# Optimization experiments

Measured on AMD Instinct MI355X. Metric: run time of the kernel, lower is better.

Reference implementation:

```python
import jax, jax.numpy as jnp
import numpy as np

B, N, C, H, D, M = 8, 4096, 512, 8, 64, 16
TOPK = 3
TAU = 0.1
DIV_REG = 0.01


def setup_inputs() -> dict:
    key = jax.random.key(0)
    ks = jax.random.split(key, 12)
    w = lambda i, shape: 0.02 * jax.random.normal(ks[i], shape, dtype=jnp.float32)
    return {
        "x": jax.random.normal(ks[0], (B, N, C), dtype=jnp.float32),
        "W_qkv": w(1, (C, 3 * C)),                    # qkv_bias=False
        "W_proj": w(2, (C, C)), "b_proj": jnp.zeros((C,), jnp.float32),
        "W_rspec": w(3, (C, H * M)), "b_rspec": jnp.zeros((H * M,), jnp.float32),
        "W_rspat": w(4, (C, H * M)), "b_rspat": jnp.zeros((H * M,), jnp.float32),
        "K_spec": w(5, (H, M, D)),                    # prototype banks (EMA buffers)
        "K_spat": w(6, (H, M, D)),
        "W_tok": w(7, (D, D)), "b_tok": jnp.zeros((D,), jnp.float32),
        "W_prot": w(8, (D, D)), "b_prot": jnp.zeros((D,), jnp.float32),
    }


def topk_mask_from_logits(logits, k):
    # keep top-k of softmax probs along last axis, renormalize
    vals = jax.lax.top_k(logits, k)[0]
    thresh = vals[..., -1:]
    mask = (logits >= thresh).astype(logits.dtype)
    probs = jax.nn.softmax(logits, axis=-1) * mask
    denom = jnp.maximum(jnp.sum(probs, axis=-1, keepdims=True), 1e-6)
    return probs / denom


def _l2norm(a, eps):
    return a / jnp.maximum(jnp.linalg.norm(a, axis=-1, keepdims=True), eps)


def reference(x, W_qkv, W_proj, b_proj, W_rspec, b_rspec, W_rspat, b_rspat,
              K_spec, K_spat, W_tok, b_tok, W_prot, b_prot):
    # qkv: [B,N,3C] -> q,k,v each [B,H,N,D]
    qkv = (x @ W_qkv).reshape(B, N, 3, H, D).transpose(2, 0, 3, 1, 4)
    q, _k, v = qkv[0], qkv[1], qkv[2]

    # routing logits [B,H,N,M] -> top-k masked probs
    r_spec = topk_mask_from_logits(
        (x @ W_rspec + b_rspec).reshape(B, N, H, M).transpose(0, 2, 1, 3), TOPK)
    r_spat = topk_mask_from_logits(
        (x @ W_rspat + b_rspat).reshape(B, N, H, M).transpose(0, 2, 1, 3), TOPK)

    # effective keys from prototype banks: [B,H,N,D]
    K_eff = (jnp.einsum('bhnm,hmd->bhnd', r_spec, K_spec)
             + jnp.einsum('bhnm,hmd->bhnd', r_spat, K_spat))
    K_norm = jax.nn.softmax(K_eff, axis=-2)          # softmax over tokens N

    # linear attention reorder: context [B,H,D,D], then Q @ context
    context = jnp.einsum('bhnd,bhne->bhde', K_norm, v)
    out = jnp.einsum('bhnd,bhde->bhne', q, context)  # note: scale unused in source
    out = out.transpose(0, 2, 1, 3).reshape(B, N, C) @ W_proj + b_proj

    # ---- contrastive aux loss ----
    t_n = _l2norm(v @ W_tok + b_tok, 1e-12)          # [B,H,N,D]
    p_spec_n = _l2norm(K_spec @ W_prot + b_prot, 1e-12)
    p_spat_n = _l2norm(K_spat @ W_prot + b_prot, 1e-12)
    sim_spec = jnp.einsum('bhnd,hmd->bhnm', t_n, p_spec_n)
    sim_spat = jnp.einsum('bhnd,hmd->bhnm', t_n, p_spat_n)
    pos_spec = jnp.sum(sim_spec * r_spec, axis=-1)
    pos_spat = jnp.sum(sim_spat * r_spat, axis=-1)
    loss_spec = -jnp.mean(pos_spec / TAU - jax.nn.logsumexp(sim_spec / TAU, axis=-1))
    loss_spat = -jnp.mean(pos_spat / TAU - jax.nn.logsumexp(sim_spat / TAU, axis=-1))
    contrastive_loss = 0.5 * (loss_spec + loss_spat)

    def diversity_loss(P):
        h, m, _d = P.shape
        p = P / jnp.maximum(jnp.linalg.norm(P, axis=-1, keepdims=True), 1e-6)
        sim = jnp.einsum('hmd,hnd->hmn', p, p)
        mask = 1.0 - jnp.eye(m, dtype=P.dtype)[None]
        return jnp.sum(sim * mask) / (h * m * (m - 1) + 1e-6)

    diversity = DIV_REG * (diversity_loss(K_spec) + diversity_loss(K_spat))
    return out, contrastive_loss, diversity
```

## Files before the change

kernel.cpp:

```cpp
#include <hip/hip_runtime.h>
#include <math.h>

#define B_ 8
#define N_ 4096
#define C_ 512
#define H_ 8
#define D_ 64
#define M_ 16
#define BN_TOK (B_*N_)
#define TAU_ 0.1f

typedef short s8v __attribute__((ext_vector_type(8)));
typedef float f4v __attribute__((ext_vector_type(4)));
typedef unsigned short u16;

__device__ __forceinline__ float wave_reduce_sum(float v){
  #pragma unroll
  for (int o = 32; o > 0; o >>= 1) v += __shfl_xor(v, o);
  return v;
}

__device__ __forceinline__ unsigned short f2b(float f){
  unsigned int u = __float_as_uint(f);
  u += 0x7fffu + ((u >> 16) & 1u);
  return (unsigned short)(u >> 16);
}

__device__ __forceinline__ float b2f(u16 b){
  return __uint_as_float(((unsigned int)b) << 16);
}

__device__ __forceinline__ s8v pack8(const float* f){
  s8v r;
  #pragma unroll
  for (int e = 0; e < 8; ++e) r[e] = (short)f2b(f[e]);
  return r;
}

__device__ __forceinline__ void gload16(const u16* g, u16* l){
  __builtin_amdgcn_global_load_lds(
      (const __attribute__((address_space(1))) unsigned int*)g,
      (__attribute__((address_space(3))) unsigned int*)l, 16, 0, 0);
}

__global__ __launch_bounds__(256) void prep_all(const float* __restrict__ x, u16* __restrict__ xb,
                                                const float* __restrict__ W_qkv,
                                                const float* __restrict__ W_rspec,
                                                const float* __restrict__ W_rspat,
                                                const float* __restrict__ W_proj,
                                                u16* __restrict__ Wqk,
                                                u16* __restrict__ Wt_v,
                                                u16* __restrict__ Wt_r,
                                                u16* __restrict__ Wt_p){
  const int bid = blockIdx.x;
  const int t = threadIdx.x;
  if (bid < 1024) {
    const int n8 = (BN_TOK*C_)/8;
    for (int i = bid * 256 + t; i < n8; i += 1024*256) {
      const float4* p = (const float4*)(x + (size_t)i * 8);
      float4 a = p[0], b = p[1];
      float f[8] = {a.x,a.y,a.z,a.w,b.x,b.y,b.z,b.w};
      *(s8v*)(xb + (size_t)i * 8) = pack8(f);
    }
    return;
  }
  if (bid < 1536) {
    const int k = bid - 1024;
    Wqk[(size_t)k*512 + t]       = f2b(W_qkv[(size_t)k*1536 + t]);
    Wqk[(size_t)k*512 + t + 256] = f2b(W_qkv[(size_t)k*1536 + t + 256]);
    return;
  }
  const int r = bid - 1536;
  const float* src; int ld, coff, n; u16* dst;
  if (r < 512)       { src = W_qkv;   ld = 1536; coff = 1024; n = r;        dst = Wt_v; }
  else if (r < 640)  { src = W_rspec; ld = 128;  coff = 0;    n = r - 512;  dst = Wt_r; }
  else if (r < 768)  { src = W_rspat; ld = 128;  coff = 0;    n = r - 640;  dst = Wt_r + 128*512; }
  else               { src = W_proj;  ld = 512;  coff = 0;    n = r - 768;  dst = Wt_p; }
  dst[(size_t)n*512 + t]       = f2b(src[(size_t)t*ld + coff + n]);
  dst[(size_t)n*512 + t + 256] = f2b(src[(size_t)(t+256)*ld + coff + n]);
}

template<int MODE>
__global__ __launch_bounds__(256) void gemm_bt(const u16* __restrict__ A,
                                               const u16* __restrict__ Bt,
                                               const float* __restrict__ bias,
                                               void* __restrict__ C,
                                               int K, int lda, int ldc, int bt_bstride) {
  __shared__ __align__(16) u16 Asm[2][2][128*32];
  __shared__ __align__(16) u16 Bsm[2][2][128*32];
  const int tid = threadIdx.x;
  const int lane = tid & 63, w = tid >> 6;
  const int bm = blockIdx.x * 128, bn = blockIdx.y * 128;

  const int lrow = lane >> 2;
  const int kch  = ((lane & 3) ^ ((lane >> 3) & 3)) << 3;

  const u16* Btb = Bt + (size_t)(bm >> 12) * bt_bstride;
  const u16* Ag0 = A   + (size_t)(bm + w*16 + lrow) * lda + kch;
  const u16* Ag1 = Ag0 + (size_t)64 * lda;
  const u16* Bg0 = Btb + (size_t)(bn + w*16 + lrow) * K + kch;
  const u16* Bg1 = Bg0 + (size_t)64 * K;
  const int l0 = (w*16)*32, l1 = (w*16+64)*32;

  const int lm = lane & 15, lg = lane >> 4;
  const int w0 = (w >> 1) * 64, c0 = (w & 1) * 64;
  const int xs = (lg ^ ((lm >> 1) & 3)) << 3;

  const int NSTEP = K >> 6;

  f4v acc[4][4];
  #pragma unroll
  for (int i = 0; i < 4; ++i)
    #pragma unroll
    for (int j = 0; j < 4; ++j) acc[i][j] = (f4v){0.f,0.f,0.f,0.f};

  #define STAGE(buf, tt)                                        \
    gload16(Ag0 + (tt)*64,      &Asm[buf][0][l0]);              \
    gload16(Ag1 + (tt)*64,      &Asm[buf][0][l1]);              \
    gload16(Ag0 + (tt)*64 + 32, &Asm[buf][1][l0]);              \
    gload16(Ag1 + (tt)*64 + 32, &Asm[buf][1][l1]);              \
    gload16(Bg0 + (tt)*64,      &Bsm[buf][0][l0]);              \
    gload16(Bg1 + (tt)*64,      &Bsm[buf][0][l1]);              \
    gload16(Bg0 + (tt)*64 + 32, &Bsm[buf][1][l0]);              \
    gload16(Bg1 + (tt)*64 + 32, &Bsm[buf][1][l1]);

  STAGE(0, 0)
  STAGE(1, 1)

  int cur = 0;
  for (int k = 0; k < NSTEP; ++k) {
    if (k < NSTEP - 1) asm volatile("s_waitcnt vmcnt(8)" ::: "memory");
    else               asm volatile("s_waitcnt vmcnt(0)" ::: "memory");
    __builtin_amdgcn_s_barrier();
    __builtin_amdgcn_sched_barrier(0);

    #pragma unroll
    for (int h = 0; h < 2; ++h) {
      s8v af[4], bf_[4];
      #pragma unroll
      for (int i = 0; i < 4; ++i) af[i]  = *(const s8v*)&Asm[cur][h][(w0 + 16*i + lm)*32 + xs];
      #pragma unroll
      for (int j = 0; j < 4; ++j) bf_[j] = *(const s8v*)&Bsm[cur][h][(c0 + 16*j + lm)*32 + xs];
      #pragma unroll
      for (int i = 0; i < 4; ++i)
        #pragma unroll
        for (int j = 0; j < 4; ++j)
          acc[i][j] = __builtin_amdgcn_mfma_f32_16x16x32_bf16(af[i], bf_[j], acc[i][j], 0, 0, 0);
    }

    __builtin_amdgcn_sched_barrier(0);
    __builtin_amdgcn_s_barrier();
    if (k + 2 < NSTEP) {
      STAGE(cur, k + 2)
    }
    __builtin_amdgcn_sched_barrier(0);
    cur ^= 1;
  }
  #undef STAGE

  #pragma unroll
  for (int j = 0; j < 4; ++j) {
    const int col = bn + c0 + 16*j + lm;
    const float bj = (MODE == 0 && bias) ? bias[col] : 0.f;
    #pragma unroll
    for (int i = 0; i < 4; ++i) {
      const int row = bm + w0 + 16*i + 4*lg;
      #pragma unroll
      for (int r = 0; r < 4; ++r) {
        if (MODE == 1) ((u16*)C)[(size_t)(row + r) * ldc + col] = f2b(acc[i][j][r]);
        else           ((float*)C)[(size_t)(row + r) * ldc + col] = acc[i][j][r] + bj;
      }
    }
  }
}

__global__ __launch_bounds__(256) void router_topk(const float* __restrict__ logits,
                            const float* __restrict__ b_rspec, const float* __restrict__ b_rspat,
                            float* __restrict__ r_spec, float* __restrict__ r_spat,
                            u16* __restrict__ rb_spec, u16* __restrict__ rb_spat) {
  int t = blockIdx.x * blockDim.x + threadIdx.x;
  if (t >= BN_TOK * H_ * 2) return;
  int route = t & 1, h = (t >> 1) & 7, bn = t >> 4;
  int b = bn >> 12, n = bn & 4095;
  const float* lg = logits + (size_t)bn*256 + route*128 + h*16;
  const float* bias = (route ? b_rspat : b_rspec) + h*16;
  float v[16];
  #pragma unroll
  for (int m=0;m<16;++m) v[m] = lg[m] + bias[m];
  float m1=-1e30f, m2=-1e30f, m3=-1e30f;
  #pragma unroll
  for (int m=0;m<16;++m){
    float x=v[m];
    if (x>m1){m3=m2;m2=m1;m1=x;}
    else if (x>m2){m3=m2;m2=x;}
    else if (x>m3){m3=x;}
  }
  float S=0.f, Sm=0.f, e[16];
  #pragma unroll
  for (int m=0;m<16;++m){ e[m]=expf(v[m]-m1); S+=e[m]; if (v[m]>=m3) Sm+=e[m]; }
  float denom = fmaxf(Sm/S, 1e-6f);
  float inv = 1.f/(S*denom);
  size_t idx = (((size_t)b*H_ + h)*N_ + n)*16;
  float* r = (route ? r_spat : r_spec) + idx;
  u16* rb  = (route ? rb_spat : rb_spec) + idx;
  #pragma unroll
  for (int m=0;m<16;++m) {
    float val = (v[m] >= m3) ? e[m]*inv : 0.f;
    r[m] = val;
    rb[m] = f2b(val);
  }
}

__global__ __launch_bounds__(256) void context_mfma(const u16* __restrict__ rb_spec, const u16* __restrict__ rb_spat,
                               const float* __restrict__ K_spec, const float* __restrict__ K_spat,
                               const u16* __restrict__ vb, float* __restrict__ pctx, float* __restrict__ pZ) {
  const int chunk = blockIdx.x & 15, bh = blockIdx.x >> 4;
  const int b = bh >> 3, h = bh & 7;
  const int tid = threadIdx.x;
  const int lane = tid & 63, w = tid >> 6;
  const int lm = lane & 15, lg = lane >> 4;

  __shared__ __align__(16) unsigned short Kc[64*32];
  __shared__ __align__(16) unsigned short Rs[64*32];
  __shared__ __align__(16) unsigned short Vt[64*64];
  __shared__ __align__(16) unsigned short Ps[64*64];
  __shared__ float Zs[256];

  {
    int d = tid & 63, c = tid >> 6;
    float f[8];
    #pragma unroll
    for (int u = 0; u < 8; ++u) {
      int k = c*8 + u;
      f[u] = (k < 16) ? K_spec[h*1024 + k*64 + d] : K_spat[h*1024 + (k-16)*64 + d];
    }
    *(s8v*)&Kc[d*32 + ((c ^ (d&3)) << 3)] = pack8(f);
  }

  const u16* rsg = rb_spec + ((size_t)bh*N_ + chunk*256)*16;
  const u16* rtg = rb_spat + ((size_t)bh*N_ + chunk*256)*16;
  const u16* vbase = vb + h*64;
  const size_t tokbase = (size_t)b*N_ + chunk*256;

  f4v acc2[4];
  #pragma unroll
  for (int j = 0; j < 4; ++j) acc2[j] = (f4v){0.f,0.f,0.f,0.f};
  float zreg[4] = {0.f,0.f,0.f,0.f};

  for (int t0 = 0; t0 < 4; ++t0) {
    __syncthreads();
    {
      int n = tid & 63, c = tid >> 6;
      const u16* src = (c < 2 ? rsg : rtg) + ((size_t)(t0*64 + n))*16 + (c&1)*8;
      *(s8v*)&Rs[n*32 + ((c ^ (n&3)) << 3)] = *(const s8v*)src;
    }
    {
      int n = tid & 63, eq = tid >> 6;
      const u16* src = vbase + (tokbase + t0*64 + n)*512 + eq*16;
      u16 f[16];
      *(s8v*)&f[0] = ((const s8v*)src)[0];
      *(s8v*)&f[8] = ((const s8v*)src)[1];
      #pragma unroll
      for (int u = 0; u < 16; ++u) {
        int e = eq*16 + u;
        Vt[e*64 + ((((n>>3) ^ (e&7)) << 3) | (n&7))] = f[u];
      }
    }
    __syncthreads();
    {
      s8v a1 = *(const s8v*)&Rs[(16*w + lm)*32 + ((lg ^ (lm&3)) << 3)];
      #pragma unroll
      for (int j = 0; j < 4; ++j) {
        s8v b1 = *(const s8v*)&Kc[(16*j + lm)*32 + ((lg ^ (lm&3)) << 3)];
        f4v c1 = (f4v){0.f,0.f,0.f,0.f};
        c1 = __builtin_amdgcn_mfma_f32_16x16x32_bf16(a1, b1, c1, 0, 0, 0);
        float p0 = expf(c1[0]), p1 = expf(c1[1]), p2 = expf(c1[2]), p3 = expf(c1[3]);
        float zz = p0 + p1 + p2 + p3;
        zz += __shfl_xor(zz, 16); zz += __shfl_xor(zz, 32);
        zreg[j] += zz;
        int d = 16*j + lm;
        int n0w = 16*w + 4*lg;
        Ps[d*64 + (((((n0w  )>>3) ^ (d&7)) << 3) | ((n0w  )&7))] = f2b(p0);
        Ps[d*64 + (((((n0w+1)>>3) ^ (d&7)) << 3) | ((n0w+1)&7))] = f2b(p1);
        Ps[d*64 + (((((n0w+2)>>3) ^ (d&7)) << 3) | ((n0w+2)&7))] = f2b(p2);
        Ps[d*64 + (((((n0w+3)>>3) ^ (d&7)) << 3) | ((n0w+3)&7))] = f2b(p3);
      }
    }
    __syncthreads();
    #pragma unroll
    for (int kb = 0; kb < 2; ++kb) {
      s8v a2 = *(const s8v*)&Vt[(16*w + lm)*64 + (((kb*4 + lg) ^ (lm&7)) << 3)];
      #pragma unroll
      for (int j = 0; j < 4; ++j) {
        s8v b2 = *(const s8v*)&Ps[(16*j + lm)*64 + (((kb*4 + lg) ^ (lm&7)) << 3)];
        acc2[j] = __builtin_amdgcn_mfma_f32_16x16x32_bf16(a2, b2, acc2[j], 0, 0, 0);
      }
    }
  }
  float* pc = pctx + (size_t)(bh*16 + chunk)*4096;
  #pragma unroll
  for (int j = 0; j < 4; ++j) {
    #pragma unroll
    for (int r = 0; r < 4; ++r)
      pc[(16*w + 4*lg + r)*64 + 16*j + lm] = acc2[j][r];
    if (lg == 0) Zs[w*64 + 16*j + lm] = zreg[j];
  }
  __syncthreads();
  if (tid < 64)
    pZ[(size_t)(bh*16 + chunk)*64 + tid] = Zs[tid] + Zs[64+tid] + Zs[128+tid] + Zs[192+tid];
}

__global__ __launch_bounds__(256) void context_reduce(const float* __restrict__ pctx, const float* __restrict__ pZ,
                              float* __restrict__ ctx) {
  const int gid = blockIdx.x * 256 + threadIdx.x;
  const int bh = gid >> 12, e = (gid >> 6) & 63, d = gid & 63;
  float z = 0.f, s = 0.f;
  for (int c = 0; c < 16; ++c) {
    z += pZ[(size_t)(bh*16 + c)*64 + d];
    s += pctx[(size_t)(bh*16 + c)*4096 + e*64 + d];
  }
  ctx[(size_t)bh*4096 + e*64 + d] = s / z;
}

__global__ __launch_bounds__(256) void cwt_kernel(const float* __restrict__ ctx, const u16* __restrict__ Wt_p,
                                                  u16* __restrict__ CWt) {
  const int bh = blockIdx.x >> 3, oct = blockIdx.x & 7;
  const int b = bh >> 3, h = bh & 7;
  const int tid = threadIdx.x;
  __shared__ float ctxS[64*64];
  __shared__ u16 WsL[64*64];
  {
    int e = tid >> 2, dq = tid & 3;
    const float4* src = (const float4*)(ctx + (size_t)bh*4096 + e*64 + dq*16);
    float4* dst = (float4*)(ctxS + e*64 + dq*16);
    dst[0] = src[0]; dst[1] = src[1]; dst[2] = src[2]; dst[3] = src[3];
  }
  const int c0 = oct * 64;
  {
    int cl = tid >> 2, eq = tid & 3;
    const s8v* src = (const s8v*)(Wt_p + (size_t)(c0 + cl)*512 + h*64 + eq*16);
    *(s8v*)&WsL[cl*64 + eq*16]     = src[0];
    *(s8v*)&WsL[cl*64 + eq*16 + 8] = src[1];
  }
  __syncthreads();
  const int d = tid & 63, cq = tid >> 6;
  for (int ci = 0; ci < 16; ++ci) {
    int cl = cq*16 + ci;
    float acc = 0.f;
    #pragma unroll
    for (int e = 0; e < 64; ++e)
      acc = fmaf(ctxS[e*64 + d], b2f(WsL[cl*64 + e]), acc);
    CWt[((size_t)b*512 + (c0 + cl))*512 + h*64 + d] = f2b(acc);
  }
}

__global__ __launch_bounds__(64) void protnorm_div(const float* __restrict__ K_spec, const float* __restrict__ K_spat,
                               const float* __restrict__ W_prot, const float* __restrict__ b_prot,
                               float* __restrict__ pnorm, float* __restrict__ pdiv) {
  const int bid = blockIdx.x;
  const int e = threadIdx.x;
  if (bid < 256) {
    int route = bid >> 7, hm = bid & 127;
    const float* Km = (route ? K_spat : K_spec) + hm*64;
    __shared__ float kv[64];
    kv[e] = Km[e];
    __syncthreads();
    float acc = b_prot[e];
    for (int dcol = 0; dcol < 64; ++dcol) acc = fmaf(kv[dcol], W_prot[dcol*64 + e], acc);
    float n2 = wave_reduce_sum(acc*acc);
    pnorm[(size_t)bid*64 + e] = acc / fmaxf(sqrtf(n2), 1e-12f);
    return;
  }
  const int db = bid - 256;
  int route = db >> 3, h = db & 7;
  const float* Km = (route ? K_spat : K_spec) + h*16*64;
  float s = 0.f, selfsum = 0.f;
  for (int m = 0; m < 16; ++m) {
    float x = Km[m*64 + e];
    float n2 = wave_reduce_sum(x*x);
    float p = x / fmaxf(sqrtf(n2), 1e-6f);
    s += p; selfsum += p*p;
  }
  float off = wave_reduce_sum(s*s - selfsum);
  if (e == 0) pdiv[db] = off;
}

__global__ __launch_bounds__(256) void contrastive_mfma(const u16* __restrict__ vb,
                                   const float* __restrict__ r_spec, const float* __restrict__ r_spat,
                                   const float* __restrict__ W_tok, const float* __restrict__ b_tok,
                                   const float* __restrict__ pnorm, float* __restrict__ pcontr) {
  const int tile = blockIdx.x & 255;
  const int h = blockIdx.x >> 8;
  const int t0 = tile * 128;
  const int b = t0 >> 12;
  const int n0 = t0 & 4095;
  const int tid = threadIdx.x;
  const int lane = tid & 63, w = tid >> 6;
  const int lm = lane & 15, lg = lane >> 4;

  __shared__ __align__(16) unsigned short Usm[128*72];
  __shared__ __align__(16) unsigned short Wsm[64*72];
  __shared__ __align__(16) unsigned short Psm[32*72];
  __shared__ float nrmS[128];
  __shared__ float btkS[64];
  __shared__ float bred[2][4];
  float* Uf = (float*)Usm;

  {
    const int vr = tid >> 1, vh = tid & 1;
    const u16* vg = vb + (size_t)(b*N_ + n0 + vr)*512 + h*64 + vh*32;
    #pragma unroll
    for (int c = 0; c < 4; ++c) *(s8v*)&Usm[vr*72 + vh*32 + c*8] = ((const s8v*)vg)[c];
  }
  {
    const int e = tid & 63, kh = tid >> 6;
    float f[16];
    #pragma unroll
    for (int rr = 0; rr < 16; ++rr) f[rr] = W_tok[(size_t)(kh*16+rr)*64 + e];
    *(s8v*)&Wsm[e*72 + kh*16]     = pack8(&f[0]);
    *(s8v*)&Wsm[e*72 + kh*16 + 8] = pack8(&f[8]);
  }
  if (tid < 128) {
    const int proto = tid >> 2, q4 = tid & 3;
    const int src = (proto < 16) ? (h*16 + proto) : (128 + h*16 + (proto-16));
    const float* pg = pnorm + (size_t)src*64 + q4*16;
    float f[16];
    #pragma unroll
    for (int i = 0; i < 4; ++i) {
      float4 v4 = ((const float4*)pg)[i];
      f[4*i]=v4.x; f[4*i+1]=v4.y; f[4*i+2]=v4.z; f[4*i+3]=v4.w;
    }
    *(s8v*)&Psm[proto*72 + q4*16]     = pack8(&f[0]);
    *(s8v*)&Psm[proto*72 + q4*16 + 8] = pack8(&f[8]);
  }
  if (tid < 64) btkS[tid] = b_tok[tid];
  __syncthreads();

  f4v acc[2][4];
  #pragma unroll
  for (int i=0;i<2;++i)
    #pragma unroll
    for (int j=0;j<4;++j) acc[i][j] = (f4v){0.f,0.f,0.f,0.f};
  {
    s8v bf0[4], bf1[4];
    #pragma unroll
    for (int j=0;j<4;++j) {
      bf0[j] = *(const s8v*)&Wsm[(j*16+lm)*72 + lg*8];
      bf1[j] = *(const s8v*)&Wsm[(j*16+lm)*72 + 32 + lg*8];
    }
    #pragma unroll
    for (int i=0;i<2;++i) {
      s8v af0 = *(const s8v*)&Usm[(w*32+16*i+lm)*72 + lg*8];
      s8v af1 = *(const s8v*)&Usm[(w*32+16*i+lm)*72 + 32 + lg*8];
      #pragma unroll
      for (int j=0;j<4;++j) {
        acc[i][j] = __builtin_amdgcn_mfma_f32_16x16x32_bf16(af0, bf0[j], acc[i][j], 0, 0, 0);
        acc[i][j] = __builtin_amdgcn_mfma_f32_16x16x32_bf16(af1, bf1[j], acc[i][j], 0, 0, 0);
      }
    }
  }
  #pragma unroll
  for (int i=0;i<2;++i) {
    #pragma unroll
    for (int r=0;r<4;++r) {
      float s = 0.f;
      #pragma unroll
      for (int j=0;j<4;++j) {
        float val = acc[i][j][r] + btkS[j*16+lm];
        acc[i][j][r] = val;
        s += val*val;
      }
      s += __shfl_xor(s,1); s += __shfl_xor(s,2); s += __shfl_xor(s,4); s += __shfl_xor(s,8);
      if (lm == 0) nrmS[w*32 + 16*i + lg*4 + r] = s;
    }
  }
  #pragma unroll
  for (int i=0;i<2;++i)
    #pragma unroll
    for (int j=0;j<4;++j)
      #pragma unroll
      for (int r=0;r<4;++r)
        Usm[(w*32+16*i+lg*4+r)*72 + j*16+lm] = f2b(acc[i][j][r]);
  __syncthreads();

  f4v acc2[2][2];
  #pragma unroll
  for (int i=0;i<2;++i)
    #pragma unroll
    for (int j=0;j<2;++j) acc2[i][j] = (f4v){0.f,0.f,0.f,0.f};
  {
    s8v bf0[2], bf1[2];
    #pragma unroll
    for (int j=0;j<2;++j) {
      bf0[j] = *(const s8v*)&Psm[(j*16+lm)*72 + lg*8];
      bf1[j] = *(const s8v*)&Psm[(j*16+lm)*72 + 32 + lg*8];
    }
    #pragma unroll
    for (int i=0;i<2;++i) {
      s8v af0 = *(const s8v*)&Usm[(w*32+16*i+lm)*72 + lg*8];
      s8v af1 = *(const s8v*)&Usm[(w*32+16*i+lm)*72 + 32 + lg*8];
      #pragma unroll
      for (int j=0;j<2;++j) {
        acc2[i][j] = __builtin_amdgcn_mfma_f32_16x16x32_bf16(af0, bf0[j], acc2[i][j], 0, 0, 0);
        acc2[i][j] = __builtin_amdgcn_mfma_f32_16x16x32_bf16(af1, bf1[j], acc2[i][j], 0, 0, 0);
      }
    }
  }
  #pragma unroll
  for (int i=0;i<2;++i)
    #pragma unroll
    for (int j=0;j<2;++j)
      #pragma unroll
      for (int r=0;r<4;++r)
        Uf[(w*32+16*i+lg*4+r)*36 + j*16+lm] = acc2[i][j][r];
  __syncthreads();

  float l = 0.f;
  {
    const int tt = tid >> 1, route = tid & 1;
    float inv = 1.f / fmaxf(sqrtf(nrmS[tt]), 1e-12f);
    const float* rg = (route ? r_spat : r_spec) + (((size_t)b*H_ + h)*N_ + n0 + tt)*16;
    float s0[16];
    #pragma unroll
    for (int m=0;m<16;++m) s0[m] = Uf[tt*36 + route*16 + m]*inv;
    float pos = 0.f, mx = -1e30f;
    #pragma unroll
    for (int m=0;m<16;++m) {
      pos += s0[m]*rg[m];
      mx = fmaxf(mx, s0[m]);
    }
    float z = 0.f;
    #pragma unroll
    for (int m=0;m<16;++m) z += expf((s0[m]-mx)/TAU_);
    l = pos/TAU_ - (mx/TAU_ + logf(z));
  }
  float lspec = (tid & 1) ? 0.f : l;
  float lspat = (tid & 1) ? l : 0.f;
  lspec = wave_reduce_sum(lspec);
  lspat = wave_reduce_sum(lspat);
  if (lane == 0) { bred[0][w]=lspec; bred[1][w]=lspat; }
  __syncthreads();
  if (tid == 0) {
    pcontr[2*blockIdx.x]     = bred[0][0]+bred[0][1]+bred[0][2]+bred[0][3];
    pcontr[2*blockIdx.x + 1] = bred[1][0]+bred[1][1]+bred[1][2]+bred[1][3];
  }
}

__global__ __launch_bounds__(256) void finalize_kernel(const float* __restrict__ pcontr,
                                                       const float* __restrict__ pdiv,
                                                       float* __restrict__ tail) {
  __shared__ float red[2][4];
  const int tid = threadIdx.x, lane = tid & 63, w = tid >> 6;
  float ls = 0.f, lt = 0.f;
  for (int k = tid; k < 2048; k += 256) { ls += pcontr[2*k]; lt += pcontr[2*k + 1]; }
  ls = wave_reduce_sum(ls);
  lt = wave_reduce_sum(lt);
  if (lane == 0) { red[0][w] = ls; red[1][w] = lt; }
  __syncthreads();
  if (tid == 0) {
    float sspec = red[0][0]+red[0][1]+red[0][2]+red[0][3];
    float sspat = red[1][0]+red[1][1]+red[1][2]+red[1][3];
    float dspec = 0.f, dspat = 0.f;
    for (int k = 0; k < 8; ++k) { dspec += pdiv[k]; dspat += pdiv[8+k]; }
    float loss_spec = -(sspec / (float)(B_*H_*N_));
    float loss_spat = -(sspat / (float)(B_*H_*N_));
    float denom = (float)(H_*M_*(M_-1)) + 1e-6f;
    tail[0] = 0.5f*(loss_spec + loss_spat);
    tail[1] = 0.01f * (dspec/denom + dspat/denom);
  }
}

extern "C" void kernel_launch(void* const* d_in, const int* in_sizes, int n_in,
                              void* d_out, int out_size, void* d_ws, size_t ws_size,
                              hipStream_t stream) {
  const float* x       = (const float*)d_in[0];
  const float* W_qkv   = (const float*)d_in[1];
  const float* W_proj  = (const float*)d_in[2];
  const float* b_proj  = (const float*)d_in[3];
  const float* W_rspec = (const float*)d_in[4];
  const float* b_rspec = (const float*)d_in[5];
  const float* W_rspat = (const float*)d_in[6];
  const float* b_rspat = (const float*)d_in[7];
  const float* K_spec  = (const float*)d_in[8];
  const float* K_spat  = (const float*)d_in[9];
  const float* W_tok   = (const float*)d_in[10];
  const float* b_tok   = (const float*)d_in[11];
  const float* W_prot  = (const float*)d_in[12];
  const float* b_prot  = (const float*)d_in[13];
  float* out = (float*)d_out;

  float* ws = (float*)d_ws;
  u16*   vb      = (u16*)ws;
  float* logits  = ws + 8388608;
  float* pctx    = ws + 8388608;
  float* pZ      = ws + 8388608 + 4194304;
  float* r_spec  = ws + 16777216;
  float* r_spat  = ws + 20971520;
  u16*   rb_spec = (u16*)(ws + 25165824);
  u16*   rb_spat = (u16*)(ws + 27262976);
  u16*   xb      = (u16*)(ws + 29360128);
  u16*   Wqk     = (u16*)(ws + 37748736);
  u16*   Wt_v    = (u16*)(ws + 37879808);
  u16*   Wt_r    = (u16*)(ws + 38010880);
  u16*   Wt_p    = (u16*)(ws + 38076416);
  float* ctxb    = ws + 38207488;
  float* pnorm   = ws + 38469632;
  float* pcontr  = ws + 38486016;
  float* pdiv    = ws + 38490112;
  u16*   CWt     = (u16*)(ws + 38490128);
  u16*   W2t     = (u16*)(ws + 39538704);

  dim3 blk256(256);

  prep_all<<<2816, blk256, 0, stream>>>(x, xb, W_qkv, W_rspec, W_rspat, W_proj, Wqk, Wt_v, Wt_r, Wt_p);

  gemm_bt<0><<<dim3(256,2), blk256, 0, stream>>>(xb, Wt_r, nullptr, logits, 512, 512, 256, 0);
  router_topk<<<2048, blk256, 0, stream>>>(logits, b_rspec, b_rspat, r_spec, r_spat, rb_spec, rb_spat);
  gemm_bt<1><<<dim3(256,4), blk256, 0, stream>>>(xb, Wt_v, nullptr, vb, 512, 512, 512, 0);
  context_mfma<<<1024, blk256, 0, stream>>>(rb_spec, rb_spat, K_spec, K_spat, vb, pctx, pZ);
  context_reduce<<<1024, blk256, 0, stream>>>(pctx, pZ, ctxb);
  cwt_kernel<<<512, blk256, 0, stream>>>(ctxb, Wt_p, CWt);
  gemm_bt<1><<<dim3(32,4), blk256, 0, stream>>>(CWt, Wqk, nullptr, W2t, 512, 512, 512, 0);
  protnorm_div<<<272, dim3(64), 0, stream>>>(K_spec, K_spat, W_prot, b_prot, pnorm, pdiv);
  contrastive_mfma<<<2048, blk256, 0, stream>>>(vb, r_spec, r_spat, W_tok, b_tok, pnorm, pcontr);
  gemm_bt<0><<<dim3(256,4), blk256, 0, stream>>>(xb, W2t, b_proj, out, 512, 512, 512, 512*512);
  finalize_kernel<<<1, blk256, 0, stream>>>(pcontr, pdiv, out + 16777216);
}
```

Baseline: 323.0 us.

## Fuse router-logit and V projections into one GEMM; drop fp32 routing probs

Adds a GEMM mode that writes the first columns of the output as bf16 V and the remaining columns as fp32 router logits, so the V projection and the router-logit projection run as one launch over a 6-column-tile grid. The router kernel no longer writes fp32 routing probabilities, and the contrastive kernel reads the bf16 copies instead. This saves a kernel launch, one pass over the activations, and a large fp32 write and read. In exchange the routing weights in the positive-similarity term now carry bf16 rounding. It also relies on the transposed router weights sitting directly after the V weights in the workspace.

```diff
diff --git a/kernel.cpp b/kernel.cpp
--- a/kernel.cpp
+++ b/kernel.cpp
@@ -85,7 +85,9 @@
                                                const u16* __restrict__ Bt,
                                                const float* __restrict__ bias,
                                                void* __restrict__ C,
-                                               int K, int lda, int ldc, int bt_bstride) {
+                                               float* __restrict__ C2,
+                                               int K, int lda, int ldc, int ldc2,
+                                               int split, int bt_bstride) {
   __shared__ __align__(16) u16 Asm[2][2][128*32];
   __shared__ __align__(16) u16 Bsm[2][2][128*32];
   const int tid = threadIdx.x;
@@ -158,6 +160,7 @@
   }
   #undef STAGE
 
+  const bool tobf = (MODE == 1) || (MODE == 2 && bn < split);
   #pragma unroll
   for (int j = 0; j < 4; ++j) {
     const int col = bn + c0 + 16*j + lm;
@@ -167,8 +170,9 @@
       const int row = bm + w0 + 16*i + 4*lg;
       #pragma unroll
       for (int r = 0; r < 4; ++r) {
-        if (MODE == 1) ((u16*)C)[(size_t)(row + r) * ldc + col] = f2b(acc[i][j][r]);
-        else           ((float*)C)[(size_t)(row + r) * ldc + col] = acc[i][j][r] + bj;
+        if (tobf)            ((u16*)C)[(size_t)(row + r) * ldc + col] = f2b(acc[i][j][r]);
+        else if (MODE == 2)  C2[(size_t)(row + r) * ldc2 + (col - split)] = acc[i][j][r];
+        else                 ((float*)C)[(size_t)(row + r) * ldc + col] = acc[i][j][r] + bj;
       }
     }
   }
@@ -176,7 +180,6 @@
 
 __global__ __launch_bounds__(256) void router_topk(const float* __restrict__ logits,
                             const float* __restrict__ b_rspec, const float* __restrict__ b_rspat,
-                            float* __restrict__ r_spec, float* __restrict__ r_spat,
                             u16* __restrict__ rb_spec, u16* __restrict__ rb_spat) {
   int t = blockIdx.x * blockDim.x + threadIdx.x;
   if (t >= BN_TOK * H_ * 2) return;
@@ -201,12 +204,10 @@
   float denom = fmaxf(Sm/S, 1e-6f);
   float inv = 1.f/(S*denom);
   size_t idx = (((size_t)b*H_ + h)*N_ + n)*16;
-  float* r = (route ? r_spat : r_spec) + idx;
   u16* rb  = (route ? rb_spat : rb_spec) + idx;
   #pragma unroll
   for (int m=0;m<16;++m) {
     float val = (v[m] >= m3) ? e[m]*inv : 0.f;
-    r[m] = val;
     rb[m] = f2b(val);
   }
 }
@@ -386,7 +387,7 @@
 }
 
 __global__ __launch_bounds__(256) void contrastive_mfma(const u16* __restrict__ vb,
-                                   const float* __restrict__ r_spec, const float* __restrict__ r_spat,
+                                   const u16* __restrict__ rb_spec, const u16* __restrict__ rb_spat,
                                    const float* __restrict__ W_tok, const float* __restrict__ b_tok,
                                    const float* __restrict__ pnorm, float* __restrict__ pcontr) {
   const int tile = blockIdx.x & 255;
@@ -519,14 +520,14 @@
   {
     const int tt = tid >> 1, route = tid & 1;
     float inv = 1.f / fmaxf(sqrtf(nrmS[tt]), 1e-12f);
-    const float* rg = (route ? r_spat : r_spec) + (((size_t)b*H_ + h)*N_ + n0 + tt)*16;
+    const u16* rg = (route ? rb_spat : rb_spec) + (((size_t)b*H_ + h)*N_ + n0 + tt)*16;
     float s0[16];
     #pragma unroll
     for (int m=0;m<16;++m) s0[m] = Uf[tt*36 + route*16 + m]*inv;
     float pos = 0.f, mx = -1e30f;
     #pragma unroll
     for (int m=0;m<16;++m) {
-      pos += s0[m]*rg[m];
+      pos += s0[m]*b2f(rg[m]);
       mx = fmaxf(mx, s0[m]);
     }
     float z = 0.f;
@@ -594,35 +595,35 @@
   float* logits  = ws + 8388608;
   float* pctx    = ws + 8388608;
   float* pZ      = ws + 8388608 + 4194304;
-  float* r_spec  = ws + 16777216;
-  float* r_spat  = ws + 20971520;
-  u16*   rb_spec = (u16*)(ws + 25165824);
-  u16*   rb_spat = (u16*)(ws + 27262976);
-  u16*   xb      = (u16*)(ws + 29360128);
-  u16*   Wqk     = (u16*)(ws + 37748736);
-  u16*   Wt_v    = (u16*)(ws + 37879808);
-  u16*   Wt_r    = (u16*)(ws + 38010880);
-  u16*   Wt_p    = (u16*)(ws + 38076416);
-  float* ctxb    = ws + 38207488;
-  float* pnorm   = ws + 38469632;
-  float* pcontr  = ws + 38486016;
-  float* pdiv    = ws + 38490112;
-  u16*   CWt     = (u16*)(ws + 38490128);
-  u16*   W2t     = (u16*)(ws + 39538704);
+  u16*   rb_spec = (u16*)(ws + 16777216);
+  u16*   rb_spat = (u16*)(ws + 18874368);
+  u16*   xb      = (u16*)(ws + 20971520);
+  u16*   Wqk     = (u16*)(ws + 29360128);
+  u16*   Wt_v    = (u16*)(ws + 29491200);
+  u16*   Wt_r    = (u16*)(ws + 29622272);
+  u16*   Wt_p    = (u16*)(ws + 29687808);
+  float* ctxb    = ws + 29818880;
+  float* pnorm   = ws + 30081024;
+  float* pcontr  = ws + 30097408;
+  float* pdiv    = ws + 30101504;
+  u16*   CWt     = (u16*)(ws + 30101520);
+  u16*   W2t     = (u16*)(ws + 31150096);
 
   dim3 blk256(256);
 
   prep_all<<<2816, blk256, 0, stream>>>(x, xb, W_qkv, W_rspec, W_rspat, W_proj, Wqk, Wt_v, Wt_r, Wt_p);
 
-  gemm_bt<0><<<dim3(256,2), blk256, 0, stream>>>(xb, Wt_r, nullptr, logits, 512, 512, 256, 0);
-  router_topk<<<2048, blk256, 0, stream>>>(logits, b_rspec, b_rspat, r_spec, r_spat, rb_spec, rb_spat);
-  gemm_bt<1><<<dim3(256,4), blk256, 0, stream>>>(xb, Wt_v, nullptr, vb, 512, 512, 512, 0);
+  gemm_bt<2><<<dim3(256,6), blk256, 0, stream>>>(xb, Wt_v, nullptr, vb, logits,
+                                                 512, 512, 512, 256, 512, 0);
+  router_topk<<<2048, blk256, 0, stream>>>(logits, b_rspec, b_rspat, rb_spec, rb_spat);
   context_mfma<<<1024, blk256, 0, stream>>>(rb_spec, rb_spat, K_spec, K_spat, vb, pctx, pZ);
   context_reduce<<<1024, blk256, 0, stream>>>(pctx, pZ, ctxb);
   cwt_kernel<<<512, blk256, 0, stream>>>(ctxb, Wt_p, CWt);
-  gemm_bt<1><<<dim3(32,4), blk256, 0, stream>>>(CWt, Wqk, nullptr, W2t, 512, 512, 512, 0);
+  gemm_bt<1><<<dim3(32,4), blk256, 0, stream>>>(CWt, Wqk, nullptr, W2t, nullptr,
+                                                512, 512, 512, 0, 1 << 30, 0);
   protnorm_div<<<272, dim3(64), 0, stream>>>(K_spec, K_spat, W_prot, b_prot, pnorm, pdiv);
-  contrastive_mfma<<<2048, blk256, 0, stream>>>(vb, r_spec, r_spat, W_tok, b_tok, pnorm, pcontr);
-  gemm_bt<0><<<dim3(256,4), blk256, 0, stream>>>(xb, W2t, b_proj, out, 512, 512, 512, 512*512);
+  contrastive_mfma<<<2048, blk256, 0, stream>>>(vb, rb_spec, rb_spat, W_tok, b_tok, pnorm, pcontr);
+  gemm_bt<0><<<dim3(256,4), blk256, 0, stream>>>(xb, W2t, b_proj, out, nullptr,
+                                                 512, 512, 512, 0, 1 << 30, 512*512);
   finalize_kernel<<<1, blk256, 0, stream>>>(pcontr, pdiv, out + 16777216);
 }
```

Measured after the change: 311.9 us. 1.04x faster.
